# Kernel optimization log

Hardware: AMD Instinct MI355X
Metric: run time of the kernel (lower is better)

## Reference

```python
import jax, jax.numpy as jnp
import numpy as np

N = 100000
E = 1600000
D = 128
BN_EPS = 1e-5


def setup_inputs() -> dict:
    key = jax.random.key(0)
    ks = jax.random.split(key, 12)
    s = 1.0 / np.sqrt(D)
    x = jax.random.normal(ks[0], (N, D), dtype=jnp.float32)
    edge_index = jax.random.randint(ks[1], (2, E), 0, N, dtype=jnp.int64)
    # Linear weights stored as [in, out] (i.e. torch W.T)
    w1a = jax.random.uniform(ks[2], (D, D), jnp.float32, -s, s)
    b1a = jax.random.uniform(ks[3], (D,), jnp.float32, -s, s)
    w1b = jax.random.uniform(ks[4], (D, D), jnp.float32, -s, s)
    b1b = jax.random.uniform(ks[5], (D,), jnp.float32, -s, s)
    gamma2 = jnp.ones((D,), jnp.float32)
    beta2 = jnp.zeros((D,), jnp.float32)
    w2a = jax.random.uniform(ks[6], (D, D), jnp.float32, -s, s)
    b2a = jax.random.uniform(ks[7], (D,), jnp.float32, -s, s)
    w2b = jax.random.uniform(ks[8], (D, D), jnp.float32, -s, s)
    b2b = jax.random.uniform(ks[9], (D,), jnp.float32, -s, s)
    return dict(x=x, edge_index=edge_index, w1a=w1a, b1a=b1a, w1b=w1b, b1b=b1b,
                gamma2=gamma2, beta2=beta2, w2a=w2a, b2a=b2a, w2b=w2b, b2b=b2b)


def _gin_conv(h, src, dst, wa, ba, wb, bb):
    # GINConv (eps=0): nn(sum_{j in N(i)} h_j + h_i), then 2-layer MLP
    agg = jax.ops.segment_sum(h[src], dst, num_segments=h.shape[0])
    z = agg + h
    z = jax.nn.relu(z @ wa + ba)
    return z @ wb + bb


def reference(x, edge_index, w1a, b1a, w1b, b1b, gamma2, beta2, w2a, b2a, w2b, b2b):
    src, dst = edge_index[0], edge_index[1]
    h = _gin_conv(x, src, dst, w1a, b1a, w1b, b1b)
    h = jax.nn.relu(h)
    # BatchNorm1d in training mode: batch mean / biased variance
    mean = jnp.mean(h, axis=0)
    var = jnp.mean((h - mean) ** 2, axis=0)
    h = (h - mean) * jax.lax.rsqrt(var + BN_EPS) * gamma2 + beta2
    return _gin_conv(h, src, dst, w2a, b2a, w2b, b2b)
```

## Files before the change

kernel.cpp:

```cpp
#include <hip/hip_runtime.h>

#define NNODES 100000
#define NEDGES 1600000
#define DIM 128
#define BN_EPS 1e-5f
#define NBUCK 1024
#define NB_USED ((NNODES + 127) / 128)
#define HISTB 128

typedef unsigned int uint;
typedef unsigned short ushort_t;
using bhalf8  = __attribute__((ext_vector_type(8))) short;
using u16x8   = __attribute__((ext_vector_type(8))) unsigned short;
using f32x4_t = __attribute__((ext_vector_type(4))) float;

__device__ __forceinline__ float bf2f(uint u16) {
    return __uint_as_float(u16 << 16);
}
__device__ __forceinline__ ushort_t f2bf(float f) {
    uint u = __float_as_uint(f);
    u += 0x7FFFu + ((u >> 16) & 1u);
    return (ushort_t)(u >> 16);
}
__device__ __forceinline__ uint pack2_bf16rn(float a, float b) {
    uint ua = __float_as_uint(a); ua += 0x7FFFu + ((ua >> 16) & 1u);
    uint ub = __float_as_uint(b); ub += 0x7FFFu + ((ub >> 16) & 1u);
    return __builtin_amdgcn_perm(ub, ua, 0x07060302u);
}

__device__ __forceinline__ int edge_src(const int* ei, int fl, int e) {
    return fl ? ei[2 * e] : ei[e];
}
__device__ __forceinline__ int edge_dst(const int* ei, int fl, int e) {
    return fl ? ei[2 * (NEDGES + e)] : ei[NEDGES + e];
}

__global__ __launch_bounds__(256) void k_prep(const float* __restrict__ X,
                                              const int* __restrict__ ei,
                                              const float* __restrict__ w0,
                                              const float* __restrict__ w1,
                                              const float* __restrict__ w2,
                                              const float* __restrict__ w3,
                                              float* __restrict__ stats,
                                              int* __restrict__ flag,
                                              int* __restrict__ parts,
                                              ushort_t* __restrict__ wbuf,
                                              ushort_t* __restrict__ Xb) {
    __shared__ int h[NBUCK];
    int bid = blockIdx.x;
    int t = threadIdx.x;
    if (bid < HISTB) {
        for (int i = t; i < NBUCK; i += 256) h[i] = 0;
        __syncthreads();
        int orr = 0;
#pragma unroll
        for (int i = 1; i < 64; i += 2) orr |= ei[i];
        int fl = (orr == 0) ? 1 : 0;
        int e0 = bid * (NEDGES / HISTB), e1 = e0 + NEDGES / HISTB;
        int e = e0 + t;
        for (; e + 768 < e1; e += 1024) {
            int d0 = edge_dst(ei, fl, e);
            int d1 = edge_dst(ei, fl, e + 256);
            int d2 = edge_dst(ei, fl, e + 512);
            int d3 = edge_dst(ei, fl, e + 768);
            atomicAdd(&h[d0 >> 7], 1);
            atomicAdd(&h[d1 >> 7], 1);
            atomicAdd(&h[d2 >> 7], 1);
            atomicAdd(&h[d3 >> 7], 1);
        }
        for (; e < e1; e += 256)
            atomicAdd(&h[edge_dst(ei, fl, e) >> 7], 1);
        __syncthreads();
        for (int i = t; i < NBUCK; i += 256) parts[bid * NBUCK + i] = h[i];
    } else if (bid < HISTB + 4) {
        int wi = bid - HISTB;
        const float* w = (wi == 0) ? w0 : (wi == 1) ? w1 : (wi == 2) ? w2 : w3;
        ushort_t* oh = wbuf + (size_t)wi * 16384;
        for (int i = t; i < 16384; i += 256) {
            int k = i >> 7, n = i & 127;
            oh[n * 128 + k] = f2bf(w[i]);
        }
    } else if (bid == HISTB + 4) {
        stats[t] = 0.0f;
        if (t == 0) {
            int orr = 0;
            for (int i = 1; i < 128; i += 2) orr |= ei[i];
            *flag = (orr == 0) ? 1 : 0;
        }
    } else {
        size_t i = ((size_t)(bid - HISTB - 5) * 256 + t) * 8;
        float4 a = *(const float4*)(X + i);
        float4 b = *(const float4*)(X + i + 4);
        union { uint4 q; u16x8 v; } o;
        o.q.x = pack2_bf16rn(a.x, a.y);
        o.q.y = pack2_bf16rn(a.z, a.w);
        o.q.z = pack2_bf16rn(b.x, b.y);
        o.q.w = pack2_bf16rn(b.z, b.w);
        *(u16x8*)(Xb + i) = o.v;
    }
}

__global__ __launch_bounds__(256) void k_bscan(const int* __restrict__ parts,
                                               int* __restrict__ bstart,
                                               int* __restrict__ bcur) {
    __shared__ int wtot[4];
    int t = threadIdx.x, lane = t & 63, w = t >> 6;
    int4 v = make_int4(0, 0, 0, 0);
    for (int b = 0; b < HISTB; ++b) {
        int4 p = ((const int4*)(parts + b * NBUCK))[t];
        v.x += p.x; v.y += p.y; v.z += p.z; v.w += p.w;
    }
    int s = v.x + v.y + v.z + v.w;
    int sc = s;
#pragma unroll
    for (int d = 1; d < 64; d <<= 1) {
        int n = __shfl_up(sc, d, 64);
        if (lane >= d) sc += n;
    }
    if (lane == 63) wtot[w] = sc;
    __syncthreads();
    int woff = 0;
    for (int i = 0; i < w; ++i) woff += wtot[i];
    int excl = woff + sc - s;
    int o0 = excl, o1 = o0 + v.x, o2 = o1 + v.y, o3 = o2 + v.z;
    bstart[t * 4]     = o0;  bcur[t * 4]     = o0;
    bstart[t * 4 + 1] = o1;  bcur[t * 4 + 1] = o1;
    bstart[t * 4 + 2] = o2;  bcur[t * 4 + 2] = o2;
    bstart[t * 4 + 3] = o3;  bcur[t * 4 + 3] = o3;
    if (t == 255) bstart[NBUCK] = o3 + v.w;
}

__global__ __launch_bounds__(256) void k_bpair(const int* __restrict__ ei,
                                               const int* __restrict__ flag,
                                               int* __restrict__ bcur,
                                               int* __restrict__ pairs) {
    __shared__ int h[NBUCK];
    __shared__ int base[NBUCK];
    int t = threadIdx.x;
    for (int i = t; i < NBUCK; i += 256) h[i] = 0;
    __syncthreads();
    int fl = *flag;
    int per = (NEDGES + gridDim.x - 1) / gridDim.x;
    int e0 = blockIdx.x * per;
    int e1 = min(e0 + per, NEDGES);
    for (int e = e0 + t; e < e1; e += 256)
        atomicAdd(&h[edge_dst(ei, fl, e) >> 7], 1);
    __syncthreads();
    for (int i = t; i < NBUCK; i += 256) {
        int c = h[i];
        base[i] = c ? atomicAdd(&bcur[i], c) : 0;
    }
    __syncthreads();
    for (int i = t; i < NBUCK; i += 256) h[i] = 0;
    __syncthreads();
    for (int e = e0 + t; e < e1; e += 256) {
        int s = edge_src(ei, fl, e);
        int d = edge_dst(ei, fl, e);
        int b = d >> 7;
        int pos = atomicAdd(&h[b], 1);
        pairs[base[b] + pos] = (s << 7) | (d & 127);
    }
}

__global__ __launch_bounds__(256) void k_bsort(const int* __restrict__ pairs,
                                               const int* __restrict__ bstart,
                                               int* __restrict__ C,
                                               int* __restrict__ ssrc) {
    __shared__ int cnt[2048];
    __shared__ int off[2048];
    __shared__ int wtot[4];
    int b = blockIdx.x;
    int t = threadIdx.x, lane = t & 63, w = t >> 6;
    int s = bstart[b], e = bstart[b + 1];
    for (int i = t; i < 2048; i += 256) cnt[i] = 0;
    __syncthreads();
    for (int i = s + t; i < e; i += 256) {
        int p = pairs[i];
        atomicAdd(&cnt[(p & 127) * 16 + (p >> 20)], 1);
    }
    __syncthreads();
    int base = t * 8, loc[8], sum = 0;
#pragma unroll
    for (int j = 0; j < 8; ++j) { loc[j] = cnt[base + j]; sum += loc[j]; }
    int sc = sum;
#pragma unroll
    for (int d = 1; d < 64; d <<= 1) {
        int n = __shfl_up(sc, d, 64);
        if (lane >= d) sc += n;
    }
    if (lane == 63) wtot[w] = sc;
    __syncthreads();
    int woff = 0;
    for (int i = 0; i < w; ++i) woff += wtot[i];
    int run = woff + sc - sum;
#pragma unroll
    for (int j = 0; j < 8; ++j) { off[base + j] = run; run += loc[j]; }
    __syncthreads();
    if (t < 128) {
        int row = b * 128 + t;
        if (row < NNODES) C[row] = s + off[t * 16 + 15] + cnt[t * 16 + 15];
    }
    __syncthreads();
    for (int i = s + t; i < e; i += 256) {
        int p = pairs[i];
        int k = (p & 127) * 16 + (p >> 20);
        int pos = atomicAdd(&off[k], 1);
        ssrc[s + pos] = p >> 7;
    }
}

template <bool BN, bool SELF_F32>
__global__ __launch_bounds__(256) void k_agg(const ushort_t* __restrict__ Xb,
                                             const float* __restrict__ Xf,
                                             ushort_t* __restrict__ Zb,
                                             const int* __restrict__ ends,
                                             const int* __restrict__ ssrc,
                                             const float* __restrict__ stats,
                                             const float* __restrict__ gamma,
                                             const float* __restrict__ beta) {
    __shared__ float scs[128], shs[128];
    int t = threadIdx.x;
    if (BN) {
        if (t < 128) {
            float s  = stats[t];
            float sq = stats[128 + t];
            float mean = s / (float)NNODES;
            float var  = sq / (float)NNODES - mean * mean;
            float sc = gamma[t] * rsqrtf(var + BN_EPS);
            scs[t] = sc;
            shs[t] = beta[t] - mean * sc;
        }
        __syncthreads();
    }
    int g = t >> 4;
    int l = t & 15;
    int row = blockIdx.x * 16 + g;
    int c8 = l * 8;
    int start = (row == 0) ? 0 : ends[row - 1];
    int end = ends[row];

    float acc[8];
    if (SELF_F32) {
        float4 a0 = *(const float4*)(Xf + (size_t)row * DIM + c8);
        float4 a1 = *(const float4*)(Xf + (size_t)row * DIM + c8 + 4);
        acc[0] = a0.x; acc[1] = a0.y; acc[2] = a0.z; acc[3] = a0.w;
        acc[4] = a1.x; acc[5] = a1.y; acc[6] = a1.z; acc[7] = a1.w;
    } else {
        union { u16x8 v; uint u[4]; } sv;
        sv.v = *(const u16x8*)(Xb + (size_t)row * DIM + c8);
#pragma unroll
        for (int i = 0; i < 4; ++i) {
            acc[2 * i]     = bf2f(sv.u[i] & 0xffffu);
            acc[2 * i + 1] = __uint_as_float(sv.u[i] & 0xffff0000u);
        }
    }

    int e = start;
    for (; e + 7 < end; e += 8) {
        union { u16x8 v; uint u[4]; } nv[8];
#pragma unroll
        for (int i = 0; i < 8; ++i) {
            int s0 = ssrc[e + i];
            nv[i].v = *(const u16x8*)(Xb + (size_t)s0 * DIM + c8);
        }
#pragma unroll
        for (int i = 0; i < 8; ++i) {
#pragma unroll
            for (int j = 0; j < 4; ++j) {
                acc[2 * j]     += bf2f(nv[i].u[j] & 0xffffu);
                acc[2 * j + 1] += __uint_as_float(nv[i].u[j] & 0xffff0000u);
            }
        }
    }
    for (; e < end; ++e) {
        int s0 = ssrc[e];
        union { u16x8 v; uint u[4]; } nv;
        nv.v = *(const u16x8*)(Xb + (size_t)s0 * DIM + c8);
#pragma unroll
        for (int j = 0; j < 4; ++j) {
            acc[2 * j]     += bf2f(nv.u[j] & 0xffffu);
            acc[2 * j + 1] += __uint_as_float(nv.u[j] & 0xffff0000u);
        }
    }

    if (BN) {
        float4 sc0 = *(const float4*)(scs + c8);
        float4 sc1 = *(const float4*)(scs + c8 + 4);
        float4 sh0 = *(const float4*)(shs + c8);
        float4 sh1 = *(const float4*)(shs + c8 + 4);
        float cnt = (float)(end - start + 1);
        acc[0] = fmaf(acc[0], sc0.x, cnt * sh0.x);
        acc[1] = fmaf(acc[1], sc0.y, cnt * sh0.y);
        acc[2] = fmaf(acc[2], sc0.z, cnt * sh0.z);
        acc[3] = fmaf(acc[3], sc0.w, cnt * sh0.w);
        acc[4] = fmaf(acc[4], sc1.x, cnt * sh1.x);
        acc[5] = fmaf(acc[5], sc1.y, cnt * sh1.y);
        acc[6] = fmaf(acc[6], sc1.z, cnt * sh1.z);
        acc[7] = fmaf(acc[7], sc1.w, cnt * sh1.w);
    }
    union { uint4 q; u16x8 v; } o;
    o.q.x = pack2_bf16rn(acc[0], acc[1]);
    o.q.y = pack2_bf16rn(acc[2], acc[3]);
    o.q.z = pack2_bf16rn(acc[4], acc[5]);
    o.q.w = pack2_bf16rn(acc[6], acc[7]);
    *(u16x8*)(Zb + (size_t)row * DIM + c8) = o.v;
}

template <bool CONV1>
__global__ __launch_bounds__(256, CONV1 ? 3 : 2)
void k_mlp(const ushort_t* __restrict__ Z,
           const ushort_t* __restrict__ WAh,
           const ushort_t* __restrict__ WBh,
           const float* __restrict__ Ba,
           const float* __restrict__ Bb,
           float* __restrict__ OutF,
           ushort_t* __restrict__ OutB,
           float* __restrict__ stats) {
    __shared__ ushort_t wsl[16384];
    __shared__ char hstage[CONV1 ? 16384 : 32768];
    __shared__ float lsum[128], lsq[128];

    int t = threadIdx.x;
    int w = t >> 6, l = t & 63;
    int lr = l & 15;
    int lg = l >> 4;
    int slane = (lr & 7) << 4;
    if (CONV1 && t < 128) { lsum[t] = 0.f; lsq[t] = 0.f; }

    int rowBase = blockIdx.x * 64 + w * 16;
    bool active = rowBase < NNODES;

#pragma unroll
    for (int i = 0; i < 8; ++i) {
        int c = i * 256 + t;
        uint4 v = ((const uint4*)WAh)[c];
        ((uint4*)wsl)[c ^ ((c >> 4) & 7)] = v;
    }
    int zrow = active ? (rowBase + lr) : 0;
    const ushort_t* zp = Z + (size_t)zrow * 128 + lg * 8;
    bhalf8 za[4];
#pragma unroll
    for (int ks = 0; ks < 4; ++ks) za[ks] = *(const bhalf8*)(zp + ks * 32);
    f32x4_t acc[8];
#pragma unroll
    for (int nt = 0; nt < 8; ++nt) {
        float b = Ba[nt * 16 + lr];
        acc[nt][0] = b; acc[nt][1] = b; acc[nt][2] = b; acc[nt][3] = b;
    }
    __syncthreads();

#pragma unroll
    for (int ks = 0; ks < 4; ++ks) {
#pragma unroll
        for (int nt = 0; nt < 8; ++nt) {
            int waddr = ((nt * 16 + lr) << 8) + ((((ks << 6) + (lg << 4))) ^ slane);
            bhalf8 wh = *(const bhalf8*)((const char*)wsl + waddr);
            acc[nt] = __builtin_amdgcn_mfma_f32_16x16x32_bf16(za[ks], wh, acc[nt], 0, 0, 0);
        }
    }
#pragma unroll
    for (int nt = 0; nt < 8; ++nt) {
#pragma unroll
        for (int j = 0; j < 4; ++j) {
            int rl = w * 16 + lg * 4 + j;
            int boff = (rl * 256 + (nt * 16 + lr) * 2) ^ ((rl & 7) << 4);
            *(ushort_t*)(hstage + boff) = f2bf(fmaxf(acc[nt][j], 0.f));
        }
    }
    __syncthreads();

#pragma unroll
    for (int i = 0; i < 8; ++i) {
        int c = i * 256 + t;
        uint4 v = ((const uint4*)WBh)[c];
        ((uint4*)wsl)[c ^ ((c >> 4) & 7)] = v;
    }
    {
        int rl = w * 16 + lr;
        int swz = (rl & 7) << 4;
#pragma unroll
        for (int ks = 0; ks < 4; ++ks)
            za[ks] = *(const bhalf8*)(hstage + ((rl * 256 + (ks * 64 + lg * 16)) ^ swz));
    }
#pragma unroll
    for (int nt = 0; nt < 8; ++nt) {
        float b = Bb[nt * 16 + lr];
        acc[nt][0] = b; acc[nt][1] = b; acc[nt][2] = b; acc[nt][3] = b;
    }
    __syncthreads();

#pragma unroll
    for (int ks = 0; ks < 4; ++ks) {
#pragma unroll
        for (int nt = 0; nt < 8; ++nt) {
            int waddr = ((nt * 16 + lr) << 8) + ((((ks << 6) + (lg << 4))) ^ slane);
            bhalf8 wh = *(const bhalf8*)((const char*)wsl + waddr);
            acc[nt] = __builtin_amdgcn_mfma_f32_16x16x32_bf16(za[ks], wh, acc[nt], 0, 0, 0);
        }
    }

    if (CONV1 && active) {
#pragma unroll
        for (int nt = 0; nt < 8; ++nt) {
            float s = 0.f, q = 0.f;
#pragma unroll
            for (int j = 0; j < 4; ++j) {
                float v = fmaxf(acc[nt][j], 0.f);
                acc[nt][j] = v;
                s += v; q += v * v;
            }
            s += __shfl_xor(s, 16); s += __shfl_xor(s, 32);
            q += __shfl_xor(q, 16); q += __shfl_xor(q, 32);
            if (l < 16) {
                atomicAdd(&lsum[nt * 16 + l], s);
                atomicAdd(&lsq[nt * 16 + l], q);
            }
        }
    }
    __syncthreads();
    if (CONV1) {
#pragma unroll
        for (int nt = 0; nt < 8; ++nt) {
#pragma unroll
            for (int j = 0; j < 4; ++j) {
                int rl = w * 16 + lg * 4 + j;
                int boff = (rl * 256 + (nt * 16 + lr) * 2) ^ ((rl & 7) << 4);
                *(ushort_t*)(hstage + boff) = f2bf(acc[nt][j]);
            }
        }
        __syncthreads();
        if (t < 128) {
            unsafeAtomicAdd(&stats[t], lsum[t]);
            unsafeAtomicAdd(&stats[128 + t], lsq[t]);
        }
        int r2 = t >> 2;
        int row = blockIdx.x * 64 + r2;
        if (row < NNODES) {
            int sw2 = (r2 & 7) << 4;
#pragma unroll
            for (int u = 0; u < 4; ++u) {
                int uu = (t & 3) * 4 + u;
                uint4 v = *(const uint4*)(hstage + ((r2 * 256 + uu * 16) ^ sw2));
                *(uint4*)(OutB + (size_t)row * 128 + uu * 8) = v;
            }
        }
    } else {
#pragma unroll
        for (int nt = 0; nt < 8; ++nt) {
#pragma unroll
            for (int j = 0; j < 4; ++j) {
                int rl = w * 16 + lg * 4 + j;
                int boff = (rl * 512 + (nt * 16 + lr) * 4) ^ ((rl & 7) << 4);
                *(float*)(hstage + boff) = acc[nt][j];
            }
        }
        __syncthreads();
        int r2 = t >> 2;
        int row = blockIdx.x * 64 + r2;
        if (row < NNODES) {
            int sw2 = (r2 & 7) << 4;
            int ch0 = (t & 3) * 8;
#pragma unroll
            for (int c = 0; c < 8; ++c) {
                float4 v = *(const float4*)(hstage + ((r2 * 512 + (ch0 + c) * 16) ^ sw2));
                *(float4*)(OutF + (size_t)row * 128 + (ch0 + c) * 4) = v;
            }
        }
    }
}

extern "C" void kernel_launch(void* const* d_in, const int* in_sizes, int n_in,
                              void* d_out, int out_size, void* d_ws, size_t ws_size,
                              hipStream_t stream) {
    const float* x     = (const float*)d_in[0];
    const int*   ei    = (const int*)d_in[1];
    const float* w1a   = (const float*)d_in[2];
    const float* b1a   = (const float*)d_in[3];
    const float* w1b   = (const float*)d_in[4];
    const float* b1b   = (const float*)d_in[5];
    const float* gamma = (const float*)d_in[6];
    const float* beta  = (const float*)d_in[7];
    const float* w2a   = (const float*)d_in[8];
    const float* b2a   = (const float*)d_in[9];
    const float* w2b   = (const float*)d_in[10];
    const float* b2b   = (const float*)d_in[11];
    float* out = (float*)d_out;

    char*     ws     = (char*)ws_size ? (char*)d_ws : (char*)d_ws;
    ws = (char*)d_ws;
    float*    stats  = (float*)ws;
    int*      flag   = (int*)(ws + 1024);
    int*      bstart = (int*)(ws + 8192);
    int*      bcur   = (int*)(ws + 16384);
    int*      C      = (int*)(ws + 404096);
    int*      ssrc   = (int*)(ws + 804096);
    ushort_t* wbuf   = (ushort_t*)(ws + 0x700000);
    int*      parts  = (int*)(ws + 0x800000);
    int*      pairs  = (int*)(ws + 0x800000);
    ushort_t* zbuf   = (ushort_t*)(ws + 0x800000);

    ushort_t* xb  = (ushort_t*)d_out;
    ushort_t* hrb = (ushort_t*)d_out + (size_t)NNODES * DIM;

    const int aggBlocks  = NNODES / 16;
    const int prepBlocks = HISTB + 5 + NNODES * DIM / (256 * 8);
    const int mlpBlocks  = (NNODES + 63) / 64;

    k_prep<<<prepBlocks, 256, 0, stream>>>(x, ei, w1a, w1b, w2a, w2b,
                                           stats, flag, parts, wbuf, xb);
    k_bscan<<<1, 256, 0, stream>>>(parts, bstart, bcur);
    k_bpair<<<256, 256, 0, stream>>>(ei, flag, bcur, pairs);
    k_bsort<<<NB_USED, 256, 0, stream>>>(pairs, bstart, C, ssrc);
    k_agg<false, true><<<aggBlocks, 256, 0, stream>>>(xb, x, zbuf, C, ssrc,
                                                      nullptr, nullptr, nullptr);
    k_mlp<true><<<mlpBlocks, 256, 0, stream>>>(
        zbuf, wbuf, wbuf + 16384, b1a, b1b, nullptr, hrb, stats);
    k_agg<true, false><<<aggBlocks, 256, 0, stream>>>(hrb, nullptr, zbuf, C, ssrc,
                                                      stats, gamma, beta);
    k_mlp<false><<<mlpBlocks, 256, 0, stream>>>(
        zbuf, wbuf + 32768, wbuf + 49152, b2a, b2b, out, nullptr, nullptr);
}
```

Before: 292.9 us.

## Fuse bucket scan into pair scatter and simplify per-bucket CSR sort

The single-block bucket scan kernel is removed. Each pair-scatter block now recomputes the global bucket offsets plus its own prefix from the per-block histograms, which doubles the histogram blocks and drops the redundant per-block recount and the global atomics on bucket cursors. The in-bucket sort now counts only by destination row (128 bins) instead of a 2048-bin row-by-source-range key. That cuts shared memory and scan work, but the source order within each row is no longer deterministic, which may hurt gather locality. The workspace layout is reshuffled to match.

```diff
diff --git a/kernel.cpp b/kernel.cpp
--- a/kernel.cpp
+++ b/kernel.cpp
@@ -6,7 +6,8 @@
 #define BN_EPS 1e-5f
 #define NBUCK 1024
 #define NB_USED ((NNODES + 127) / 128)
-#define HISTB 128
+#define HISTB 256
+#define EPB (NEDGES / HISTB)
 
 typedef unsigned int uint;
 typedef unsigned short ushort_t;
@@ -56,7 +57,7 @@
 #pragma unroll
         for (int i = 1; i < 64; i += 2) orr |= ei[i];
         int fl = (orr == 0) ? 1 : 0;
-        int e0 = bid * (NEDGES / HISTB), e1 = e0 + NEDGES / HISTB;
+        int e0 = bid * EPB, e1 = e0 + EPB;
         int e = e0 + t;
         for (; e + 768 < e1; e += 1024) {
             int d0 = edge_dst(ei, fl, e);
@@ -100,17 +101,23 @@
     }
 }
 
-__global__ __launch_bounds__(256) void k_bscan(const int* __restrict__ parts,
+__global__ __launch_bounds__(256) void k_bpair(const int* __restrict__ ei,
+                                               const int* __restrict__ flag,
+                                               const int* __restrict__ parts,
                                                int* __restrict__ bstart,
-                                               int* __restrict__ bcur) {
+                                               int* __restrict__ pairs) {
+    __shared__ int cur[NBUCK];
     __shared__ int wtot[4];
-    int t = threadIdx.x, lane = t & 63, w = t >> 6;
-    int4 v = make_int4(0, 0, 0, 0);
-    for (int b = 0; b < HISTB; ++b) {
-        int4 p = ((const int4*)(parts + b * NBUCK))[t];
-        v.x += p.x; v.y += p.y; v.z += p.z; v.w += p.w;
-    }
-    int s = v.x + v.y + v.z + v.w;
+    int k = blockIdx.x, t = threadIdx.x;
+    int lane = t & 63, w = t >> 6;
+    int4 pre = make_int4(0, 0, 0, 0);
+    int4 tot = make_int4(0, 0, 0, 0);
+    for (int kk = 0; kk < HISTB; ++kk) {
+        int4 v = ((const int4*)(parts + kk * NBUCK))[t];
+        if (kk < k) { pre.x += v.x; pre.y += v.y; pre.z += v.z; pre.w += v.w; }
+        tot.x += v.x; tot.y += v.y; tot.z += v.z; tot.w += v.w;
+    }
+    int s = tot.x + tot.y + tot.z + tot.w;
     int sc = s;
 #pragma unroll
     for (int d = 1; d < 64; d <<= 1) {
@@ -122,43 +129,27 @@
     int woff = 0;
     for (int i = 0; i < w; ++i) woff += wtot[i];
     int excl = woff + sc - s;
-    int o0 = excl, o1 = o0 + v.x, o2 = o1 + v.y, o3 = o2 + v.z;
-    bstart[t * 4]     = o0;  bcur[t * 4]     = o0;
-    bstart[t * 4 + 1] = o1;  bcur[t * 4 + 1] = o1;
-    bstart[t * 4 + 2] = o2;  bcur[t * 4 + 2] = o2;
-    bstart[t * 4 + 3] = o3;  bcur[t * 4 + 3] = o3;
-    if (t == 255) bstart[NBUCK] = o3 + v.w;
-}
-
-__global__ __launch_bounds__(256) void k_bpair(const int* __restrict__ ei,
-                                               const int* __restrict__ flag,
-                                               int* __restrict__ bcur,
-                                               int* __restrict__ pairs) {
-    __shared__ int h[NBUCK];
-    __shared__ int base[NBUCK];
-    int t = threadIdx.x;
-    for (int i = t; i < NBUCK; i += 256) h[i] = 0;
+    int b0 = excl, b1 = b0 + tot.x, b2 = b1 + tot.y, b3 = b2 + tot.z;
+    cur[t * 4]     = b0 + pre.x;
+    cur[t * 4 + 1] = b1 + pre.y;
+    cur[t * 4 + 2] = b2 + pre.z;
+    cur[t * 4 + 3] = b3 + pre.w;
+    if (k == 0) {
+        bstart[t * 4]     = b0;
+        bstart[t * 4 + 1] = b1;
+        bstart[t * 4 + 2] = b2;
+        bstart[t * 4 + 3] = b3;
+        if (t == 255) bstart[NBUCK] = b3 + tot.w;
+    }
     __syncthreads();
     int fl = *flag;
-    int per = (NEDGES + gridDim.x - 1) / gridDim.x;
-    int e0 = blockIdx.x * per;
-    int e1 = min(e0 + per, NEDGES);
-    for (int e = e0 + t; e < e1; e += 256)
-        atomicAdd(&h[edge_dst(ei, fl, e) >> 7], 1);
-    __syncthreads();
-    for (int i = t; i < NBUCK; i += 256) {
-        int c = h[i];
-        base[i] = c ? atomicAdd(&bcur[i], c) : 0;
-    }
-    __syncthreads();
-    for (int i = t; i < NBUCK; i += 256) h[i] = 0;
-    __syncthreads();
+    int e0 = k * EPB, e1 = e0 + EPB;
     for (int e = e0 + t; e < e1; e += 256) {
-        int s = edge_src(ei, fl, e);
+        int src = edge_src(ei, fl, e);
         int d = edge_dst(ei, fl, e);
         int b = d >> 7;
-        int pos = atomicAdd(&h[b], 1);
-        pairs[base[b] + pos] = (s << 7) | (d & 127);
+        int pos = atomicAdd(&cur[b], 1);
+        pairs[pos] = (src << 7) | (d & 127);
     }
 }
 
@@ -166,45 +157,38 @@
                                                const int* __restrict__ bstart,
                                                int* __restrict__ C,
                                                int* __restrict__ ssrc) {
-    __shared__ int cnt[2048];
-    __shared__ int off[2048];
-    __shared__ int wtot[4];
+    __shared__ int cnt[128];
+    __shared__ int off[128];
     int b = blockIdx.x;
     int t = threadIdx.x, lane = t & 63, w = t >> 6;
     int s = bstart[b], e = bstart[b + 1];
-    for (int i = t; i < 2048; i += 256) cnt[i] = 0;
+    if (t < 128) cnt[t] = 0;
+    __syncthreads();
+    for (int i = s + t; i < e; i += 256)
+        atomicAdd(&cnt[pairs[i] & 127], 1);
+    __syncthreads();
+    if (w == 0) {
+        int c0 = cnt[lane], c1 = cnt[64 + lane];
+        int s0 = c0, s1 = c1;
+#pragma unroll
+        for (int d = 1; d < 64; d <<= 1) {
+            int n0 = __shfl_up(s0, d, 64);
+            int n1 = __shfl_up(s1, d, 64);
+            if (lane >= d) { s0 += n0; s1 += n1; }
+        }
+        int tot0 = __shfl(s0, 63, 64);
+        off[lane]      = s0 - c0;
+        off[64 + lane] = tot0 + s1 - c1;
+    }
+    __syncthreads();
+    if (t < 128) {
+        int row = b * 128 + t;
+        if (row < NNODES) C[row] = s + off[t] + cnt[t];
+    }
     __syncthreads();
     for (int i = s + t; i < e; i += 256) {
         int p = pairs[i];
-        atomicAdd(&cnt[(p & 127) * 16 + (p >> 20)], 1);
-    }
-    __syncthreads();
-    int base = t * 8, loc[8], sum = 0;
-#pragma unroll
-    for (int j = 0; j < 8; ++j) { loc[j] = cnt[base + j]; sum += loc[j]; }
-    int sc = sum;
-#pragma unroll
-    for (int d = 1; d < 64; d <<= 1) {
-        int n = __shfl_up(sc, d, 64);
-        if (lane >= d) sc += n;
-    }
-    if (lane == 63) wtot[w] = sc;
-    __syncthreads();
-    int woff = 0;
-    for (int i = 0; i < w; ++i) woff += wtot[i];
-    int run = woff + sc - sum;
-#pragma unroll
-    for (int j = 0; j < 8; ++j) { off[base + j] = run; run += loc[j]; }
-    __syncthreads();
-    if (t < 128) {
-        int row = b * 128 + t;
-        if (row < NNODES) C[row] = s + off[t * 16 + 15] + cnt[t * 16 + 15];
-    }
-    __syncthreads();
-    for (int i = s + t; i < e; i += 256) {
-        int p = pairs[i];
-        int k = (p & 127) * 16 + (p >> 20);
-        int pos = atomicAdd(&off[k], 1);
+        int pos = atomicAdd(&off[p & 127], 1);
         ssrc[s + pos] = p >> 7;
     }
 }
@@ -486,18 +470,16 @@
     const float* b2b   = (const float*)d_in[11];
     float* out = (float*)d_out;
 
-    char*     ws     = (char*)ws_size ? (char*)d_ws : (char*)d_ws;
-    ws = (char*)d_ws;
+    char* ws = (char*)d_ws;
     float*    stats  = (float*)ws;
     int*      flag   = (int*)(ws + 1024);
     int*      bstart = (int*)(ws + 8192);
-    int*      bcur   = (int*)(ws + 16384);
-    int*      C      = (int*)(ws + 404096);
-    int*      ssrc   = (int*)(ws + 804096);
-    ushort_t* wbuf   = (ushort_t*)(ws + 0x700000);
-    int*      parts  = (int*)(ws + 0x800000);
-    int*      pairs  = (int*)(ws + 0x800000);
-    ushort_t* zbuf   = (ushort_t*)(ws + 0x800000);
+    int*      parts  = (int*)(ws + 0x10000);
+    int*      C      = (int*)(ws + 0x180000);
+    int*      ssrc   = (int*)(ws + 0x200000);
+    ushort_t* wbuf   = (ushort_t*)(ws + 0x900000);
+    int*      pairs  = (int*)(ws + 0xA00000);
+    ushort_t* zbuf   = (ushort_t*)(ws + 0xA00000);
 
     ushort_t* xb  = (ushort_t*)d_out;
     ushort_t* hrb = (ushort_t*)d_out + (size_t)NNODES * DIM;
@@ -508,8 +490,7 @@
 
     k_prep<<<prepBlocks, 256, 0, stream>>>(x, ei, w1a, w1b, w2a, w2b,
                                            stats, flag, parts, wbuf, xb);
-    k_bscan<<<1, 256, 0, stream>>>(parts, bstart, bcur);
-    k_bpair<<<256, 256, 0, stream>>>(ei, flag, bcur, pairs);
+    k_bpair<<<HISTB, 256, 0, stream>>>(ei, flag, parts, bstart, pairs);
     k_bsort<<<NB_USED, 256, 0, stream>>>(pairs, bstart, C, ssrc);
     k_agg<false, true><<<aggBlocks, 256, 0, stream>>>(xb, x, zbuf, C, ssrc,
                                                       nullptr, nullptr, nullptr);
```

Measured after the change: 304.7 us. 1.04x slower.
